# Kernel optimization log

Measured on AMD Instinct MI355X. Metric: run time of the kernel, lower is better.

Reference implementation:

```python
import jax, jax.numpy as jnp
import numpy as np

D, H, L, P, NQ, B, DFF = 256, 8, 4, 5, 900, 8, 1024
DH = D // H
SHAPES = np.array([[128, 128], [64, 64], [32, 32], [16, 16]], dtype=np.int64)
S = int((SHAPES[:, 0] * SHAPES[:, 1]).sum())  # 21760
EPS = 1e-5


def layer_norm(x, g, b):
    m = jnp.mean(x, -1, keepdims=True)
    v = jnp.mean((x - m) ** 2, -1, keepdims=True)
    return (x - m) * jax.lax.rsqrt(v + EPS) * g + b


def bilerp(v2, x, y, Wl, Hl):
    # v2: [BH, Hl, Wl, Dh]; x, y: [BH, N] pixel coords (align_corners=False)
    x0 = jnp.floor(x); y0 = jnp.floor(y)
    fx = x - x0; fy = y - y0
    x0i = x0.astype(jnp.int32); y0i = y0.astype(jnp.int32)
    bidx = jnp.arange(v2.shape[0])[:, None]
    out = jnp.zeros(x.shape + (v2.shape[-1],), v2.dtype)
    for dy in (0, 1):
        for dx in (0, 1):
            xi = x0i + dx; yi = y0i + dy
            w = (fx if dx else 1.0 - fx) * (fy if dy else 1.0 - fy)
            valid = (xi >= 0) & (xi < Wl) & (yi >= 0) & (yi < Hl)
            xc = jnp.clip(xi, 0, Wl - 1); yc = jnp.clip(yi, 0, Hl - 1)
            out = out + (w * valid)[..., None] * v2[bidx, yc, xc]
    return out


def setup_inputs() -> dict:
    key = jax.random.key(0)
    ks = jax.random.split(key, 32)
    p = lambda i, shp: (jax.random.normal(ks[i], shp, jnp.float32) * 0.02)
    inp = {
        'tgt': jax.random.normal(ks[0], (NQ, B, D), jnp.float32),
        'tgt_query_pos': jax.random.normal(ks[1], (NQ, B, D), jnp.float32),
        'tgt_reference_points': jax.random.uniform(ks[2], (NQ, B, L, 4), jnp.float32),
        'memory': jax.random.normal(ks[3], (S, B, D), jnp.float32),
        'sa_in_w': p(4, (3 * D, D)), 'sa_in_b': jnp.zeros((3 * D,)),
        'sa_out_w': p(5, (D, D)), 'sa_out_b': jnp.zeros((D,)),
        'off_w': p(6, (H * L * P * 2, D)), 'off_b': jax.random.uniform(ks[7], (H * L * P * 2,), jnp.float32, -1.0, 1.0),
        'aw_w': p(8, (H * L * P, D)), 'aw_b': jnp.zeros((H * L * P,)),
        'val_w': p(9, (D, D)), 'val_b': jnp.zeros((D,)),
        'co_w': p(10, (D, D)), 'co_b': jnp.zeros((D,)),
        'w1': p(11, (DFF, D)), 'b1': jnp.zeros((DFF,)),
        'w2': p(12, (D, DFF)), 'b2': jnp.zeros((D,)),
        'ln1_g': jnp.ones((D,)), 'ln1_b': jnp.zeros((D,)),
        'ln2_g': jnp.ones((D,)), 'ln2_b': jnp.zeros((D,)),
        'ln3_g': jnp.ones((D,)), 'ln3_b': jnp.zeros((D,)),
        'memory_spatial_shapes': np.array(SHAPES),
        'memory_level_start_index': np.concatenate([[0], np.cumsum(SHAPES[:, 0] * SHAPES[:, 1])[:-1]]),
    }
    return inp


def reference(tgt, tgt_query_pos, tgt_reference_points, memory,
              sa_in_w, sa_in_b, sa_out_w, sa_out_b,
              off_w, off_b, aw_w, aw_b, val_w, val_b, co_w, co_b,
              w1, b1, w2, b2, ln1_g, ln1_b, ln2_g, ln2_b, ln3_g, ln3_b,
              memory_spatial_shapes, memory_level_start_index):
    shapes = np.asarray(memory_spatial_shapes)

    # ---- self-attention (norm2) ----
    q = tgt + tgt_query_pos  # [nq,B,D], k == q, v == tgt
    qp = (q @ sa_in_w[:D].T + sa_in_b[:D]).reshape(NQ, B, H, DH)
    kp = (q @ sa_in_w[D:2 * D].T + sa_in_b[D:2 * D]).reshape(NQ, B, H, DH)
    vp = (tgt @ sa_in_w[2 * D:].T + sa_in_b[2 * D:]).reshape(NQ, B, H, DH)
    scores = jnp.einsum('qbhd,kbhd->bhqk', qp, kp) / jnp.sqrt(jnp.float32(DH))
    attn = jax.nn.softmax(scores, -1)
    sa = jnp.einsum('bhqk,kbhd->qbhd', attn, vp).reshape(NQ, B, D)
    sa = sa @ sa_out_w.T + sa_out_b
    tgt = layer_norm(tgt + sa, ln2_g, ln2_b)

    # ---- deformable cross-attention (norm1) ----
    query = (tgt + tgt_query_pos).transpose(1, 0, 2)          # [B,nq,D]
    value = (memory.transpose(1, 0, 2) @ val_w.T + val_b).reshape(B, S, H, DH)
    offsets = (query @ off_w.T + off_b).reshape(B, NQ, H, L, P, 2)
    aw = (query @ aw_w.T + aw_b).reshape(B, NQ, H, L * P)
    aw = jax.nn.softmax(aw, -1).reshape(B, NQ, H, L, P)
    ref = tgt_reference_points.transpose(1, 0, 2, 3)          # [B,nq,L,4]
    locs = ref[:, :, None, :, None, :2] + offsets / P * ref[:, :, None, :, None, 2:] * 0.5

    acc = jnp.zeros((B, H, NQ, DH), jnp.float32)
    start = 0
    for l in range(L):
        Hl, Wl = int(shapes[l, 0]), int(shapes[l, 1])
        v2 = value[:, start:start + Hl * Wl].reshape(B, Hl, Wl, H, DH)
        v2 = v2.transpose(0, 3, 1, 2, 4).reshape(B * H, Hl, Wl, DH)
        loc = locs[:, :, :, l].transpose(0, 2, 1, 3, 4).reshape(B * H, NQ * P, 2)
        x = loc[..., 0] * Wl - 0.5
        y = loc[..., 1] * Hl - 0.5
        samp = bilerp(v2, x, y, Wl, Hl).reshape(B, H, NQ, P, DH)
        w_l = aw[:, :, :, l].transpose(0, 2, 1, 3)            # [B,H,nq,P]
        acc = acc + jnp.einsum('bhqp,bhqpd->bhqd', w_l, samp)
        start += Hl * Wl
    ca = acc.transpose(0, 2, 1, 3).reshape(B, NQ, D) @ co_w.T + co_b
    tgt = layer_norm(tgt + ca.transpose(1, 0, 2), ln1_g, ln1_b)

    # ---- FFN (norm3) ----
    h = jax.nn.relu(tgt @ w1.T + b1) @ w2.T + b2
    tgt = layer_norm(tgt + h, ln3_g, ln3_b)
    return tgt
```

## Files before the change

### kernel.cpp

```cpp
#include <hip/hip_runtime.h>
#include <hip/hip_bf16.h>

#define NQ   900
#define BB   8
#define DD   256
#define HH   8
#define DH   32
#define LL   4
#define PP   5
#define SS   21760
#define DFF  1024
#define MQ   (NQ*BB)
#define MV   (SS*BB)

typedef __bf16 bf16_t;
typedef __bf16 bf16x8 __attribute__((ext_vector_type(8)));
typedef __bf16 bf16x4 __attribute__((ext_vector_type(4)));
typedef float  f32x4  __attribute__((ext_vector_type(4)));

__device__ __forceinline__ void async16(const void* g, void* l) {
  __builtin_amdgcn_global_load_lds(
      (const __attribute__((address_space(1))) unsigned int*)g,
      (__attribute__((address_space(3))) unsigned int*)l, 16, 0, 0);
}

template<typename AT, int EPI, typename OT>
__global__ __launch_bounds__(256) void gemm128(
    const AT* __restrict__ A, const bf16_t* __restrict__ W,
    const float* __restrict__ bias, OT* __restrict__ C,
    int M, int N, int K, int tiles_n)
{
  constexpr bool AF = (sizeof(AT) == 4);
  __shared__ __align__(16) AT     As[128 * 32];
  __shared__ __align__(16) bf16_t Bs[128 * 32];
  const int tm = blockIdx.x / tiles_n;
  const int tn = blockIdx.x - tm * tiles_n;
  const int m0 = tm << 7, n0 = tn << 7;
  const int t = threadIdx.x;
  const int wave = t >> 6, lane = t & 63;
  const int wr = wave >> 1, wc = wave & 1;
  const int lm = lane & 15, kq = lane >> 4;

  f32x4 acc[4][4];
#pragma unroll
  for (int i = 0; i < 4; ++i)
#pragma unroll
    for (int j = 0; j < 4; ++j) acc[i][j] = (f32x4){0.f, 0.f, 0.f, 0.f};

  for (int k0 = 0; k0 < K; k0 += 32) {
    __syncthreads();
    if constexpr (AF) {
#pragma unroll
      for (int i = 0; i < 4; ++i) {
        int flat = i * 4096 + t * 16;
        int row = flat >> 7;
        int cl = (flat >> 4) & 7;
        int cg = cl ^ (row & 7);
        int grow = m0 + row; if (grow >= M) grow = M - 1;
        async16(&A[(size_t)grow * K + k0 + cg * 4], (char*)As + flat);
      }
    } else {
#pragma unroll
      for (int i = 0; i < 2; ++i) {
        int flat = i * 4096 + t * 16;
        int row = flat >> 6;
        int cl = (flat >> 4) & 3;
        int cg = cl ^ ((row >> 1) & 3);
        int grow = m0 + row; if (grow >= M) grow = M - 1;
        async16(&A[(size_t)grow * K + k0 + cg * 8], (char*)As + flat);
      }
    }
#pragma unroll
    for (int i = 0; i < 2; ++i) {
      int flat = i * 4096 + t * 16;
      int row = flat >> 6;
      int cl = (flat >> 4) & 3;
      int cg = cl ^ ((row >> 1) & 3);
      int grow = n0 + row; if (grow >= N) grow = N - 1;
      async16(&W[(size_t)grow * K + k0 + cg * 8], (char*)Bs + flat);
    }
    __syncthreads();

    bf16x8 af[4], bfr[4];
#pragma unroll
    for (int mi = 0; mi < 4; ++mi) {
      int row = wr * 64 + mi * 16 + lm;
      if constexpr (AF) {
        int s = row & 7;
        const float* rp = (const float*)As + row * 32;
        f32x4 lo = *(const f32x4*)(rp + (((2 * kq) ^ s) << 2));
        f32x4 hi = *(const f32x4*)(rp + (((2 * kq + 1) ^ s) << 2));
        bf16x8 f;
#pragma unroll
        for (int j = 0; j < 4; ++j) { f[j] = (bf16_t)lo[j]; f[4 + j] = (bf16_t)hi[j]; }
        af[mi] = f;
      } else {
        int s = (row >> 1) & 3;
        af[mi] = *(const bf16x8*)((const bf16_t*)As + row * 32 + ((kq ^ s) << 3));
      }
    }
#pragma unroll
    for (int ni = 0; ni < 4; ++ni) {
      int row = wc * 64 + ni * 16 + lm;
      int s = (row >> 1) & 3;
      bfr[ni] = *(const bf16x8*)(Bs + row * 32 + ((kq ^ s) << 3));
    }
#pragma unroll
    for (int mi = 0; mi < 4; ++mi)
#pragma unroll
      for (int ni = 0; ni < 4; ++ni)
        acc[mi][ni] = __builtin_amdgcn_mfma_f32_16x16x32_bf16(af[mi], bfr[ni], acc[mi][ni], 0, 0, 0);
  }

  const int colb = n0 + wc * 64 + lm;
  float bv[4]; bool cok[4];
#pragma unroll
  for (int ni = 0; ni < 4; ++ni) {
    int c = colb + ni * 16;
    cok[ni] = (c < N);
    bv[ni] = cok[ni] ? bias[c] : 0.f;
  }
#pragma unroll
  for (int mi = 0; mi < 4; ++mi) {
    int rbase = m0 + wr * 64 + mi * 16 + kq * 4;
#pragma unroll
    for (int reg = 0; reg < 4; ++reg) {
      int r = rbase + reg;
      if (r < M) {
#pragma unroll
        for (int ni = 0; ni < 4; ++ni) if (cok[ni]) {
          float v = acc[mi][ni][reg] + bv[ni];
          if (EPI == 1) v = fmaxf(v, 0.f);
          C[(size_t)r * N + colb + ni * 16] = (OT)v;
        }
      }
    }
  }
}

__global__ __launch_bounds__(256) void cvt_kernel(
    const float* __restrict__ in, bf16_t* __restrict__ out, int n8)
{
  int i = blockIdx.x * 256 + threadIdx.x;
  if (i < n8) {
    f32x4 x0 = ((const f32x4*)in)[2 * i], x1 = ((const f32x4*)in)[2 * i + 1];
    bf16x8 r;
#pragma unroll
    for (int j = 0; j < 4; ++j) { r[j] = (bf16_t)x0[j]; r[4 + j] = (bf16_t)x1[j]; }
    ((bf16x8*)out)[i] = r;
  }
}

__global__ __launch_bounds__(256) void addpos_kernel(
    const float* __restrict__ a, const float* __restrict__ b,
    bf16_t* __restrict__ o, int n8)
{
  int i = blockIdx.x * 256 + threadIdx.x;
  if (i < n8) {
    f32x4 x0 = ((const f32x4*)a)[2 * i], x1 = ((const f32x4*)a)[2 * i + 1];
    f32x4 y0 = ((const f32x4*)b)[2 * i], y1 = ((const f32x4*)b)[2 * i + 1];
    bf16x8 r;
#pragma unroll
    for (int j = 0; j < 4; ++j) { r[j] = (bf16_t)(x0[j] + y0[j]); r[4 + j] = (bf16_t)(x1[j] + y1[j]); }
    ((bf16x8*)o)[i] = r;
  }
}

template<int WBF>
__global__ __launch_bounds__(256) void lnres_kernel(
    const float* __restrict__ x, const float* __restrict__ res,
    const float* __restrict__ g, const float* __restrict__ bta,
    float* __restrict__ out, bf16_t* __restrict__ outb, int rows)
{
  int wave = threadIdx.x >> 6, lane = threadIdx.x & 63;
  int row = blockIdx.x * 4 + wave;
  if (row >= rows) return;
  const float4* xp = (const float4*)(x + (size_t)row * DD);
  const float4* rp = (const float4*)(res + (size_t)row * DD);
  float4 v = xp[lane], rr = rp[lane];
  float a0 = v.x + rr.x, a1 = v.y + rr.y, a2 = v.z + rr.z, a3 = v.w + rr.w;
  float s = a0 + a1 + a2 + a3;
#pragma unroll
  for (int off = 32; off; off >>= 1) s += __shfl_xor(s, off);
  float mean = s * (1.0f / DD);
  float d0 = a0 - mean, d1 = a1 - mean, d2 = a2 - mean, d3 = a3 - mean;
  float vs = d0 * d0 + d1 * d1 + d2 * d2 + d3 * d3;
#pragma unroll
  for (int off = 32; off; off >>= 1) vs += __shfl_xor(vs, off);
  float inv = rsqrtf(vs * (1.0f / DD) + 1e-5f);
  float4 gg = ((const float4*)g)[lane];
  float4 bb = ((const float4*)bta)[lane];
  float o0 = d0 * inv * gg.x + bb.x, o1 = d1 * inv * gg.y + bb.y;
  float o2 = d2 * inv * gg.z + bb.z, o3 = d3 * inv * gg.w + bb.w;
  float4 o; o.x = o0; o.y = o1; o.z = o2; o.w = o3;
  ((float4*)(out + (size_t)row * DD))[lane] = o;
  if (WBF) {
    bf16x4 ob; ob[0] = (bf16_t)o0; ob[1] = (bf16_t)o1; ob[2] = (bf16_t)o2; ob[3] = (bf16_t)o3;
    ((bf16x4*)(outb + (size_t)row * DD))[lane] = ob;
  }
}

__global__ __launch_bounds__(256) void attn_mfma(
    const bf16_t* __restrict__ qk, const bf16_t* __restrict__ vp,
    bf16_t* __restrict__ sa)
{
  __shared__ __align__(16) bf16_t Ks[128 * 32];
  __shared__ __align__(16) bf16_t VT[32 * 136];
  __shared__ __align__(16) bf16_t Pw[4][16 * 136];
  const int bh = blockIdx.x;
  const int b = bh & 7, h = bh >> 3;
  const int qt = blockIdx.y;
  const int t = threadIdx.x, wave = t >> 6, lane = t & 63;
  const int lm = lane & 15, quad = lane >> 4;
  const int q0 = qt * 64 + wave * 16;

  int qrow = q0 + lm; if (qrow > NQ - 1) qrow = NQ - 1;
  bf16x8 aqr = *(const bf16x8*)&qk[((size_t)qrow * BB + b) * 512 + h * 32 + quad * 8];
  bf16x8 aq;
#pragma unroll
  for (int j = 0; j < 8; ++j) aq[j] = (bf16_t)((float)aqr[j] * 0.17677669529663687f);

  f32x4 m_run = {-1e30f, -1e30f, -1e30f, -1e30f};
  f32x4 l_run = {0.f, 0.f, 0.f, 0.f};
  f32x4 o0 = {0.f, 0.f, 0.f, 0.f}, o1 = {0.f, 0.f, 0.f, 0.f};
  const f32x4 zero = {0.f, 0.f, 0.f, 0.f};

  for (int c = 0; c < 8; ++c) {
    const int k0 = c * 128;
    __syncthreads();
#pragma unroll
    for (int i = 0; i < 2; ++i) {
      int flat = i * 4096 + t * 16;
      int row = flat >> 6;
      int cl = (flat >> 4) & 3;
      int cg = cl ^ ((row >> 1) & 3);
      int key = k0 + row; if (key > NQ - 1) key = NQ - 1;
      async16(&qk[((size_t)key * BB + b) * 512 + 256 + h * 32 + cg * 8], (char*)Ks + flat);
    }
#pragma unroll
    for (int i = 0; i < 2; ++i) {
      int idx = t * 2 + i;
      int key = idx >> 2, dc = idx & 3;
      int gk = k0 + key;
      if (gk < NQ) {
        bf16x8 vv = *(const bf16x8*)&vp[((size_t)gk * BB + b) * 256 + h * 32 + dc * 8];
#pragma unroll
        for (int u = 0; u < 8; ++u) VT[(dc * 8 + u) * 136 + key] = vv[u];
      } else {
#pragma unroll
        for (int u = 0; u < 8; ++u) VT[(dc * 8 + u) * 136 + key] = (bf16_t)0.f;
      }
    }
    __syncthreads();

    f32x4 s[8];
#pragma unroll
    for (int blk = 0; blk < 8; ++blk) {
      int row = blk * 16 + lm;
      int sw = (row >> 1) & 3;
      bf16x8 kb = *(const bf16x8*)&Ks[row * 32 + ((quad ^ sw) << 3)];
      s[blk] = __builtin_amdgcn_mfma_f32_16x16x32_bf16(aq, kb, zero, 0, 0, 0);
    }
    if (c == 7) {
#pragma unroll
      for (int blk = 0; blk < 8; ++blk) {
        if (k0 + blk * 16 + lm >= NQ) {
#pragma unroll
          for (int r = 0; r < 4; ++r) s[blk][r] = -1e30f;
        }
      }
    }
    f32x4 mx = s[0];
#pragma unroll
    for (int blk = 1; blk < 8; ++blk)
#pragma unroll
      for (int r = 0; r < 4; ++r) mx[r] = fmaxf(mx[r], s[blk][r]);
#pragma unroll
    for (int d = 1; d < 16; d <<= 1)
#pragma unroll
      for (int r = 0; r < 4; ++r) mx[r] = fmaxf(mx[r], __shfl_xor(mx[r], d));
    f32x4 m_new, alpha;
#pragma unroll
    for (int r = 0; r < 4; ++r) {
      m_new[r] = fmaxf(m_run[r], mx[r]);
      alpha[r] = __expf(m_run[r] - m_new[r]);
    }
    f32x4 psum = {0.f, 0.f, 0.f, 0.f};
#pragma unroll
    for (int blk = 0; blk < 8; ++blk) {
#pragma unroll
      for (int r = 0; r < 4; ++r) {
        float p = __expf(s[blk][r] - m_new[r]);
        psum[r] += p;
        Pw[wave][(quad * 4 + r) * 136 + blk * 16 + lm] = (bf16_t)p;
      }
    }
#pragma unroll
    for (int d = 1; d < 16; d <<= 1)
#pragma unroll
      for (int r = 0; r < 4; ++r) psum[r] += __shfl_xor(psum[r], d);
#pragma unroll
    for (int r = 0; r < 4; ++r) {
      l_run[r] = l_run[r] * alpha[r] + psum[r];
      m_run[r] = m_new[r];
      o0[r] *= alpha[r];
      o1[r] *= alpha[r];
    }
    bf16x8 ap[4];
#pragma unroll
    for (int kc = 0; kc < 4; ++kc)
      ap[kc] = *(const bf16x8*)&Pw[wave][lm * 136 + kc * 32 + quad * 8];
#pragma unroll
    for (int kc = 0; kc < 4; ++kc) {
      bf16x8 vb0 = *(const bf16x8*)&VT[lm * 136 + kc * 32 + quad * 8];
      bf16x8 vb1 = *(const bf16x8*)&VT[(16 + lm) * 136 + kc * 32 + quad * 8];
      o0 = __builtin_amdgcn_mfma_f32_16x16x32_bf16(ap[kc], vb0, o0, 0, 0, 0);
      o1 = __builtin_amdgcn_mfma_f32_16x16x32_bf16(ap[kc], vb1, o1, 0, 0, 0);
    }
  }
#pragma unroll
  for (int r = 0; r < 4; ++r) {
    int q = q0 + quad * 4 + r;
    if (q < NQ) {
      float inv = 1.0f / l_run[r];
      size_t base = ((size_t)q * BB + b) * 256 + h * 32;
      sa[base + lm] = (bf16_t)(o0[r] * inv);
      sa[base + 16 + lm] = (bf16_t)(o1[r] * inv);
    }
  }
}

__global__ __launch_bounds__(256) void deform_kernel(
    const bf16_t* __restrict__ value, const float* __restrict__ offs,
    const float* __restrict__ awl, const float* __restrict__ refp,
    bf16_t* __restrict__ out)
{
  __shared__ float logits[160];
  __shared__ float wfin[160][4];
  __shared__ int   tidx[160][4];
  __shared__ float hmax[8], hsum[8];
  const int r = blockIdx.x;
  const int b = r & 7;
  const int t = threadIdx.x;
  if (t < 160) {
    int i20 = t % 20;
    int l = i20 / 5;
    logits[t] = awl[(size_t)r * 160 + t];
    float ox = offs[(size_t)r * 320 + t * 2];
    float oy = offs[(size_t)r * 320 + t * 2 + 1];
    const float* rp = refp + ((size_t)r * LL + l) * 4;
    int Wl = 128 >> l;
    int st = (l == 0) ? 0 : (l == 1) ? 16384 : (l == 2) ? 20480 : 21504;
    float lx = rp[0] + ox * 0.1f * rp[2];
    float ly = rp[1] + oy * 0.1f * rp[3];
    float xx = lx * (float)Wl - 0.5f;
    float yy = ly * (float)Wl - 0.5f;
    float x0f = floorf(xx), y0f = floorf(yy);
    float fx = xx - x0f, fy = yy - y0f;
    int x0 = (int)x0f, y0 = (int)y0f;
#pragma unroll
    for (int tap = 0; tap < 4; ++tap) {
      int dx = tap & 1, dy = tap >> 1;
      int xi = x0 + dx, yi = y0 + dy;
      float w = (dx ? fx : 1.0f - fx) * (dy ? fy : 1.0f - fy);
      bool valid = (xi >= 0) & (xi < Wl) & (yi >= 0) & (yi < Wl);
      int xc = min(max(xi, 0), Wl - 1);
      int yc = min(max(yi, 0), Wl - 1);
      tidx[t][tap] = (st + yc * Wl + xc) * BB + b;
      wfin[t][tap] = valid ? w : 0.0f;
    }
  }
  __syncthreads();
  if (t < 8) {
    float m = -1e30f;
    for (int i = 0; i < 20; ++i) m = fmaxf(m, logits[t * 20 + i]);
    float s = 0.f;
    for (int i = 0; i < 20; ++i) s += __expf(logits[t * 20 + i] - m);
    hmax[t] = m; hsum[t] = s;
  }
  __syncthreads();
  if (t < 160) {
    int h = t / 20;
    float p = __expf(logits[t] - hmax[h]) / hsum[h];
#pragma unroll
    for (int tap = 0; tap < 4; ++tap) wfin[t][tap] *= p;
  }
  __syncthreads();
  const int h = t >> 5, d = t & 31;
  const bf16_t* vbase = value + h * 32 + d;
  float acc = 0.f;
#pragma unroll 4
  for (int i = 0; i < 20; ++i) {
    int e = h * 20 + i;
#pragma unroll
    for (int tap = 0; tap < 4; ++tap) {
      float w = wfin[e][tap];
      float v = (float)vbase[(size_t)tidx[e][tap] * 256];
      acc = fmaf(w, v, acc);
    }
  }
  out[(size_t)r * 256 + t] = (bf16_t)acc;
}

static inline int tiles(int x) { return (x + 127) >> 7; }

extern "C" void kernel_launch(void* const* d_in, const int* in_sizes, int n_in,
                              void* d_out, int out_size, void* d_ws, size_t ws_size,
                              hipStream_t stream) {
  const float* tgt     = (const float*)d_in[0];
  const float* pos     = (const float*)d_in[1];
  const float* refp    = (const float*)d_in[2];
  const float* memory  = (const float*)d_in[3];
  const float* sa_in_w = (const float*)d_in[4];
  const float* sa_in_b = (const float*)d_in[5];
  const float* sa_out_w= (const float*)d_in[6];
  const float* sa_out_b= (const float*)d_in[7];
  const float* off_w   = (const float*)d_in[8];
  const float* off_b   = (const float*)d_in[9];
  const float* aw_w    = (const float*)d_in[10];
  const float* aw_b    = (const float*)d_in[11];
  const float* val_w   = (const float*)d_in[12];
  const float* val_b   = (const float*)d_in[13];
  const float* co_w    = (const float*)d_in[14];
  const float* co_b    = (const float*)d_in[15];
  const float* w1      = (const float*)d_in[16];
  const float* b1      = (const float*)d_in[17];
  const float* w2      = (const float*)d_in[18];
  const float* b2      = (const float*)d_in[19];
  const float* ln1_g   = (const float*)d_in[20];
  const float* ln1_b   = (const float*)d_in[21];
  const float* ln2_g   = (const float*)d_in[22];
  const float* ln2_b   = (const float*)d_in[23];
  const float* ln3_g   = (const float*)d_in[24];
  const float* ln3_b   = (const float*)d_in[25];

  char* ws = (char*)d_ws;
  bf16_t* value_bf = (bf16_t*)ws;
  bf16_t* qk_bf    = (bf16_t*)(ws + 89128960);
  bf16_t* h1_bf    = qk_bf;
  bf16_t* qsum_bf  = (bf16_t*)(ws + 103874560);
  bf16_t* vp_bf    = (bf16_t*)(ws + 107560960);
  bf16_t* sa_bf    = (bf16_t*)(ws + 111247360);
  float*  tgt2     = (float*)(ws + 114933760);
  bf16_t* query_bf = (bf16_t*)(ws + 122306560);
  float*  offs     = (float*)(ws + 125992960);
  float*  awl      = (float*)(ws + 135208960);
  bf16_t* ca_bf    = (bf16_t*)(ws + 139816960);
  float*  gout     = (float*)(ws + 143503360);
  float*  tgt3     = (float*)(ws + 150876160);
  bf16_t* tgt3_bf  = (bf16_t*)(ws + 158248960);
  bf16_t* wbf      = (bf16_t*)(ws + 161935360);
  bf16_t* sa_in_wb = wbf;
  bf16_t* sa_out_wb= wbf + 196608;
  bf16_t* off_wb   = wbf + 262144;
  bf16_t* aw_wb    = wbf + 344064;
  bf16_t* val_wb   = wbf + 385024;
  bf16_t* co_wb    = wbf + 450560;
  bf16_t* w1b      = wbf + 516096;
  bf16_t* w2b      = wbf + 778240;
  float*  outp     = (float*)d_out;

  const int n8q = MQ * DD / 8;

  auto cvt = [&](const float* in, bf16_t* out, int n) {
    int n8 = n / 8;
    cvt_kernel<<<dim3((n8 + 255) / 256), 256, 0, stream>>>(in, out, n8);
  };
  cvt(sa_in_w, sa_in_wb, 196608);
  cvt(sa_out_w, sa_out_wb, 65536);
  cvt(off_w, off_wb, 81920);
  cvt(aw_w, aw_wb, 40960);
  cvt(val_w, val_wb, 65536);
  cvt(co_w, co_wb, 65536);
  cvt(w1, w1b, 262144);
  cvt(w2, w2b, 262144);

  addpos_kernel<<<dim3((n8q + 255) / 256), 256, 0, stream>>>(tgt, pos, qsum_bf, n8q);
  gemm128<bf16_t, 0, bf16_t><<<dim3(tiles(MQ) * 4), 256, 0, stream>>>(
      qsum_bf, sa_in_wb, sa_in_b, qk_bf, MQ, 512, 256, 4);
  gemm128<float, 0, bf16_t><<<dim3(tiles(MQ) * 2), 256, 0, stream>>>(
      tgt, sa_in_wb + 512 * 256, sa_in_b + 512, vp_bf, MQ, 256, 256, 2);
  attn_mfma<<<dim3(64, 15), 256, 0, stream>>>(qk_bf, vp_bf, sa_bf);
  gemm128<bf16_t, 0, float><<<dim3(tiles(MQ) * 2), 256, 0, stream>>>(
      sa_bf, sa_out_wb, sa_out_b, gout, MQ, 256, 256, 2);
  lnres_kernel<0><<<dim3((MQ + 3) / 4), 256, 0, stream>>>(
      gout, tgt, ln2_g, ln2_b, tgt2, (bf16_t*)nullptr, MQ);

  addpos_kernel<<<dim3((n8q + 255) / 256), 256, 0, stream>>>(tgt2, pos, query_bf, n8q);
  gemm128<float, 0, bf16_t><<<dim3(tiles(MV) * 2), 256, 0, stream>>>(
      memory, val_wb, val_b, value_bf, MV, 256, 256, 2);
  gemm128<bf16_t, 0, float><<<dim3(tiles(MQ) * 3), 256, 0, stream>>>(
      query_bf, off_wb, off_b, offs, MQ, 320, 256, 3);
  gemm128<bf16_t, 0, float><<<dim3(tiles(MQ) * 2), 256, 0, stream>>>(
      query_bf, aw_wb, aw_b, awl, MQ, 160, 256, 2);
  deform_kernel<<<dim3(MQ), 256, 0, stream>>>(value_bf, offs, awl, refp, ca_bf);
  gemm128<bf16_t, 0, float><<<dim3(tiles(MQ) * 2), 256, 0, stream>>>(
      ca_bf, co_wb, co_b, gout, MQ, 256, 256, 2);
  lnres_kernel<1><<<dim3((MQ + 3) / 4), 256, 0, stream>>>(
      gout, tgt2, ln1_g, ln1_b, tgt3, tgt3_bf, MQ);

  gemm128<bf16_t, 1, bf16_t><<<dim3(tiles(MQ) * 8), 256, 0, stream>>>(
      tgt3_bf, w1b, b1, h1_bf, MQ, DFF, 256, 8);
  gemm128<bf16_t, 0, float><<<dim3(tiles(MQ) * 2), 256, 0, stream>>>(
      h1_bf, w2b, b2, gout, MQ, 256, DFF, 2);
  lnres_kernel<0><<<dim3((MQ + 3) / 4), 256, 0, stream>>>(
      gout, tgt3, ln3_g, ln3_b, outp, (bf16_t*)nullptr, MQ);

  (void)in_sizes; (void)n_in; (void)out_size; (void)ws_size;
}
```

Baseline: 629.3 us.

## Add K=256 GEMM with full weight panel in LDS and direct A loads

Adds a new GEMM kernel for K=256 projections. It keeps a 64-column by full-K weight panel resident in swizzled LDS, streams A rows straight from global memory into registers (converting fp32 to bf16 on the fly), and stages bf16 outputs through LDS for vectorized stores. All K=256 projections, including the large value projection over memory, now use it, and the fp32-A path is removed from gemm128. The eight weight-conversion launches are merged into a single kernel. The intent is to cut per-k-step barriers, LDS traffic for A, and launch overhead, at the cost of uncached, uncoalesced-per-wave A reads and a 32 KB LDS footprint per block.

```diff
diff --git a/kernel.cpp b/kernel.cpp
--- a/kernel.cpp
+++ b/kernel.cpp
@@ -24,14 +24,129 @@
       (__attribute__((address_space(3))) unsigned int*)l, 16, 0, 0);
 }
 
+template<typename AT, typename OT, int RELU>
+__global__ __launch_bounds__(256) void vgemm(
+    const AT* __restrict__ A, const bf16_t* __restrict__ W,
+    const float* __restrict__ bias, OT* __restrict__ C,
+    int M, int N, int nt)
+{
+  constexpr bool AF = (sizeof(AT) == 4);
+  __shared__ __align__(16) bf16_t Ws[64 * 256];
+  const int blk = blockIdx.x;
+  const int tn = blk % nt, tm = blk / nt;
+  const int n0 = tn << 6, m0 = tm << 8;
+  const int t = threadIdx.x, wave = t >> 6, lane = t & 63;
+  const int lm = lane & 15, quad = lane >> 4;
+
+#pragma unroll
+  for (int j = 0; j < 8; ++j) {
+    int flat = j * 4096 + t * 16;
+    int col = flat >> 9;
+    int kc = ((flat >> 4) & 31) ^ (col & 31);
+    int colg = n0 + col; if (colg >= N) colg = N - 1;
+    async16(&W[(size_t)colg * 256 + kc * 8], (char*)Ws + flat);
+  }
+  __syncthreads();
+
+  f32x4 acc[4][4];
+#pragma unroll
+  for (int i = 0; i < 4; ++i)
+#pragma unroll
+    for (int j = 0; j < 4; ++j) acc[i][j] = (f32x4){0.f, 0.f, 0.f, 0.f};
+
+#pragma unroll 2
+  for (int k0 = 0; k0 < 256; k0 += 32) {
+    const int ki = k0 >> 3;
+    bf16x8 bfr[4];
+#pragma unroll
+    for (int ni = 0; ni < 4; ++ni) {
+      int col = ni * 16 + lm;
+      int ch = (ki + quad) ^ (col & 31);
+      bfr[ni] = *(const bf16x8*)&Ws[col * 256 + ch * 8];
+    }
+    bf16x8 af[4];
+#pragma unroll
+    for (int mi = 0; mi < 4; ++mi) {
+      int row = m0 + wave * 64 + mi * 16 + lm; if (row >= M) row = M - 1;
+      if constexpr (AF) {
+        const float* ap = A + (size_t)row * 256 + k0 + quad * 8;
+        f32x4 lo = *(const f32x4*)ap;
+        f32x4 hi = *(const f32x4*)(ap + 4);
+        bf16x8 f;
+#pragma unroll
+        for (int j = 0; j < 4; ++j) { f[j] = (bf16_t)lo[j]; f[4 + j] = (bf16_t)hi[j]; }
+        af[mi] = f;
+      } else {
+        af[mi] = *(const bf16x8*)&A[(size_t)row * 256 + k0 + quad * 8];
+      }
+    }
+#pragma unroll
+    for (int mi = 0; mi < 4; ++mi)
+#pragma unroll
+      for (int ni = 0; ni < 4; ++ni)
+        acc[mi][ni] = __builtin_amdgcn_mfma_f32_16x16x32_bf16(af[mi], bfr[ni], acc[mi][ni], 0, 0, 0);
+  }
+
+  float bv[4];
+#pragma unroll
+  for (int ni = 0; ni < 4; ++ni) {
+    int c = n0 + ni * 16 + lm;
+    bv[ni] = (c < N) ? bias[c] : 0.f;
+  }
+
+  if constexpr (sizeof(OT) == 4) {
+#pragma unroll
+    for (int mi = 0; mi < 4; ++mi) {
+#pragma unroll
+      for (int r = 0; r < 4; ++r) {
+        int row = m0 + wave * 64 + mi * 16 + quad * 4 + r;
+        if (row < M) {
+#pragma unroll
+          for (int ni = 0; ni < 4; ++ni) {
+            int col = n0 + ni * 16 + lm;
+            if (col < N) {
+              float v = acc[mi][ni][r] + bv[ni];
+              if (RELU) v = fmaxf(v, 0.f);
+              C[(size_t)row * N + col] = (OT)v;
+            }
+          }
+        }
+      }
+    }
+  } else {
+    __syncthreads();
+    bf16_t* Os = Ws;
+#pragma unroll
+    for (int mi = 0; mi < 4; ++mi)
+#pragma unroll
+      for (int r = 0; r < 4; ++r) {
+        int rl = wave * 64 + mi * 16 + quad * 4 + r;
+#pragma unroll
+        for (int ni = 0; ni < 4; ++ni) {
+          float v = acc[mi][ni][r] + bv[ni];
+          if (RELU) v = fmaxf(v, 0.f);
+          Os[rl * 64 + ni * 16 + lm] = (bf16_t)v;
+        }
+      }
+    __syncthreads();
+#pragma unroll
+    for (int i = 0; i < 8; ++i) {
+      int fe = i * 2048 + t * 8;
+      int rl = fe >> 6, cl = fe & 63;
+      int row = m0 + rl, colg = n0 + cl;
+      if (row < M && colg < N)
+        *(bf16x8*)&C[(size_t)row * N + colg] = *(const bf16x8*)&Os[fe];
+    }
+  }
+}
+
 template<typename AT, int EPI, typename OT>
 __global__ __launch_bounds__(256) void gemm128(
     const AT* __restrict__ A, const bf16_t* __restrict__ W,
     const float* __restrict__ bias, OT* __restrict__ C,
     int M, int N, int K, int tiles_n)
 {
-  constexpr bool AF = (sizeof(AT) == 4);
-  __shared__ __align__(16) AT     As[128 * 32];
+  __shared__ __align__(16) bf16_t As[128 * 32];
   __shared__ __align__(16) bf16_t Bs[128 * 32];
   const int tm = blockIdx.x / tiles_n;
   const int tn = blockIdx.x - tm * tiles_n;
@@ -49,26 +164,14 @@
 
   for (int k0 = 0; k0 < K; k0 += 32) {
     __syncthreads();
-    if constexpr (AF) {
-#pragma unroll
-      for (int i = 0; i < 4; ++i) {
-        int flat = i * 4096 + t * 16;
-        int row = flat >> 7;
-        int cl = (flat >> 4) & 7;
-        int cg = cl ^ (row & 7);
-        int grow = m0 + row; if (grow >= M) grow = M - 1;
-        async16(&A[(size_t)grow * K + k0 + cg * 4], (char*)As + flat);
-      }
-    } else {
-#pragma unroll
-      for (int i = 0; i < 2; ++i) {
-        int flat = i * 4096 + t * 16;
-        int row = flat >> 6;
-        int cl = (flat >> 4) & 3;
-        int cg = cl ^ ((row >> 1) & 3);
-        int grow = m0 + row; if (grow >= M) grow = M - 1;
-        async16(&A[(size_t)grow * K + k0 + cg * 8], (char*)As + flat);
-      }
+#pragma unroll
+    for (int i = 0; i < 2; ++i) {
+      int flat = i * 4096 + t * 16;
+      int row = flat >> 6;
+      int cl = (flat >> 4) & 3;
+      int cg = cl ^ ((row >> 1) & 3);
+      int grow = m0 + row; if (grow >= M) grow = M - 1;
+      async16(&A[(size_t)grow * K + k0 + cg * 8], (char*)As + flat);
     }
 #pragma unroll
     for (int i = 0; i < 2; ++i) {
@@ -85,19 +188,8 @@
 #pragma unroll
     for (int mi = 0; mi < 4; ++mi) {
       int row = wr * 64 + mi * 16 + lm;
-      if constexpr (AF) {
-        int s = row & 7;
-        const float* rp = (const float*)As + row * 32;
-        f32x4 lo = *(const f32x4*)(rp + (((2 * kq) ^ s) << 2));
-        f32x4 hi = *(const f32x4*)(rp + (((2 * kq + 1) ^ s) << 2));
-        bf16x8 f;
-#pragma unroll
-        for (int j = 0; j < 4; ++j) { f[j] = (bf16_t)lo[j]; f[4 + j] = (bf16_t)hi[j]; }
-        af[mi] = f;
-      } else {
-        int s = (row >> 1) & 3;
-        af[mi] = *(const bf16x8*)((const bf16_t*)As + row * 32 + ((kq ^ s) << 3));
-      }
+      int s = (row >> 1) & 3;
+      af[mi] = *(const bf16x8*)((const bf16_t*)As + row * 32 + ((kq ^ s) << 3));
     }
 #pragma unroll
     for (int ni = 0; ni < 4; ++ni) {
@@ -138,17 +230,30 @@
   }
 }
 
-__global__ __launch_bounds__(256) void cvt_kernel(
-    const float* __restrict__ in, bf16_t* __restrict__ out, int n8)
+__global__ __launch_bounds__(256) void cvt_all(
+    const float* __restrict__ s0, const float* __restrict__ s1,
+    const float* __restrict__ s2, const float* __restrict__ s3,
+    const float* __restrict__ s4, const float* __restrict__ s5,
+    const float* __restrict__ s6, const float* __restrict__ s7,
+    bf16_t* __restrict__ dst)
 {
   int i = blockIdx.x * 256 + threadIdx.x;
-  if (i < n8) {
-    f32x4 x0 = ((const f32x4*)in)[2 * i], x1 = ((const f32x4*)in)[2 * i + 1];
-    bf16x8 r;
-#pragma unroll
-    for (int j = 0; j < 4; ++j) { r[j] = (bf16_t)x0[j]; r[4 + j] = (bf16_t)x1[j]; }
-    ((bf16x8*)out)[i] = r;
-  }
+  if (i >= 130048) return;
+  const float* s; int base;
+  if (i < 24576)      { s = s0; base = 0; }
+  else if (i < 32768) { s = s1; base = 24576; }
+  else if (i < 43008) { s = s2; base = 32768; }
+  else if (i < 48128) { s = s3; base = 43008; }
+  else if (i < 56320) { s = s4; base = 48128; }
+  else if (i < 64512) { s = s5; base = 56320; }
+  else if (i < 97280) { s = s6; base = 64512; }
+  else                { s = s7; base = 97280; }
+  int li = i - base;
+  f32x4 x0 = ((const f32x4*)s)[2 * li], x1 = ((const f32x4*)s)[2 * li + 1];
+  bf16x8 r;
+#pragma unroll
+  for (int j = 0; j < 4; ++j) { r[j] = (bf16_t)x0[j]; r[4 + j] = (bf16_t)x1[j]; }
+  ((bf16x8*)dst)[i] = r;
 }
 
 __global__ __launch_bounds__(256) void addpos_kernel(
@@ -461,46 +566,37 @@
   float*  outp     = (float*)d_out;
 
   const int n8q = MQ * DD / 8;
-
-  auto cvt = [&](const float* in, bf16_t* out, int n) {
-    int n8 = n / 8;
-    cvt_kernel<<<dim3((n8 + 255) / 256), 256, 0, stream>>>(in, out, n8);
-  };
-  cvt(sa_in_w, sa_in_wb, 196608);
-  cvt(sa_out_w, sa_out_wb, 65536);
-  cvt(off_w, off_wb, 81920);
-  cvt(aw_w, aw_wb, 40960);
-  cvt(val_w, val_wb, 65536);
-  cvt(co_w, co_wb, 65536);
-  cvt(w1, w1b, 262144);
-  cvt(w2, w2b, 262144);
+  const int mtq = (MQ + 255) >> 8;
+
+  cvt_all<<<dim3(508), 256, 0, stream>>>(
+      sa_in_w, sa_out_w, off_w, aw_w, val_w, co_w, w1, w2, wbf);
 
   addpos_kernel<<<dim3((n8q + 255) / 256), 256, 0, stream>>>(tgt, pos, qsum_bf, n8q);
-  gemm128<bf16_t, 0, bf16_t><<<dim3(tiles(MQ) * 4), 256, 0, stream>>>(
-      qsum_bf, sa_in_wb, sa_in_b, qk_bf, MQ, 512, 256, 4);
-  gemm128<float, 0, bf16_t><<<dim3(tiles(MQ) * 2), 256, 0, stream>>>(
-      tgt, sa_in_wb + 512 * 256, sa_in_b + 512, vp_bf, MQ, 256, 256, 2);
+  vgemm<bf16_t, bf16_t, 0><<<dim3(mtq * 8), 256, 0, stream>>>(
+      qsum_bf, sa_in_wb, sa_in_b, qk_bf, MQ, 512, 8);
+  vgemm<float, bf16_t, 0><<<dim3(mtq * 4), 256, 0, stream>>>(
+      tgt, sa_in_wb + 512 * 256, sa_in_b + 512, vp_bf, MQ, 256, 4);
   attn_mfma<<<dim3(64, 15), 256, 0, stream>>>(qk_bf, vp_bf, sa_bf);
-  gemm128<bf16_t, 0, float><<<dim3(tiles(MQ) * 2), 256, 0, stream>>>(
-      sa_bf, sa_out_wb, sa_out_b, gout, MQ, 256, 256, 2);
+  vgemm<bf16_t, float, 0><<<dim3(mtq * 4), 256, 0, stream>>>(
+      sa_bf, sa_out_wb, sa_out_b, gout, MQ, 256, 4);
   lnres_kernel<0><<<dim3((MQ + 3) / 4), 256, 0, stream>>>(
       gout, tgt, ln2_g, ln2_b, tgt2, (bf16_t*)nullptr, MQ);
 
   addpos_kernel<<<dim3((n8q + 255) / 256), 256, 0, stream>>>(tgt2, pos, query_bf, n8q);
-  gemm128<float, 0, bf16_t><<<dim3(tiles(MV) * 2), 256, 0, stream>>>(
-      memory, val_wb, val_b, value_bf, MV, 256, 256, 2);
-  gemm128<bf16_t, 0, float><<<dim3(tiles(MQ) * 3), 256, 0, stream>>>(
-      query_bf, off_wb, off_b, offs, MQ, 320, 256, 3);
-  gemm128<bf16_t, 0, float><<<dim3(tiles(MQ) * 2), 256, 0, stream>>>(
-      query_bf, aw_wb, aw_b, awl, MQ, 160, 256, 2);
+  vgemm<float, bf16_t, 0><<<dim3(680 * 4), 256, 0, stream>>>(
+      memory, val_wb, val_b, value_bf, MV, 256, 4);
+  vgemm<bf16_t, float, 0><<<dim3(mtq * 5), 256, 0, stream>>>(
+      query_bf, off_wb, off_b, offs, MQ, 320, 5);
+  vgemm<bf16_t, float, 0><<<dim3(mtq * 3), 256, 0, stream>>>(
+      query_bf, aw_wb, aw_b, awl, MQ, 160, 3);
   deform_kernel<<<dim3(MQ), 256, 0, stream>>>(value_bf, offs, awl, refp, ca_bf);
-  gemm128<bf16_t, 0, float><<<dim3(tiles(MQ) * 2), 256, 0, stream>>>(
-      ca_bf, co_wb, co_b, gout, MQ, 256, 256, 2);
+  vgemm<bf16_t, float, 0><<<dim3(mtq * 4), 256, 0, stream>>>(
+      ca_bf, co_wb, co_b, gout, MQ, 256, 4);
   lnres_kernel<1><<<dim3((MQ + 3) / 4), 256, 0, stream>>>(
       gout, tgt2, ln1_g, ln1_b, tgt3, tgt3_bf, MQ);
 
-  gemm128<bf16_t, 1, bf16_t><<<dim3(tiles(MQ) * 8), 256, 0, stream>>>(
-      tgt3_bf, w1b, b1, h1_bf, MQ, DFF, 256, 8);
+  vgemm<bf16_t, bf16_t, 1><<<dim3(mtq * 16), 256, 0, stream>>>(
+      tgt3_bf, w1b, b1, h1_bf, MQ, 1024, 16);
   gemm128<bf16_t, 0, float><<<dim3(tiles(MQ) * 2), 256, 0, stream>>>(
       h1_bf, w2b, b2, gout, MQ, 256, DFF, 2);
   lnres_kernel<0><<<dim3((MQ + 3) / 4), 256, 0, stream>>>(
```

Measured after the change: 608.7 us. 1.03x faster.
